# Optimization experiments

Hardware: AMD Instinct MI355X
Metric: run time of the kernel (lower is better)

Reference implementation:

```python
import jax, jax.numpy as jnp
import numpy as np

GROUP_SIZE = 128

def _dequantize(qweight, wscales, wzeros):
    # qweight: [N, K//2] packed bytes, two uint4 values per byte
    # low nibble = even k index, high nibble = odd k index
    N, Kh = qweight.shape
    K = Kh * 2
    low = qweight & 0xF
    high = (qweight >> 4) & 0xF
    w_int = jnp.stack([low, high], axis=-1).reshape(N, K).astype(jnp.float32)  # [N, K]
    G = K // GROUP_SIZE  # number of groups along K
    w_grp = w_int.reshape(N, G, GROUP_SIZE)
    s = wscales.T.reshape(N, G, 1)   # wscales: [G, N] -> [N, G, 1]
    z = wzeros.T.reshape(N, G, 1)
    return ((w_grp - z) * s).reshape(N, K)  # [N, K] dequantized

def setup_inputs() -> dict:
    key = jax.random.key(0)
    k1, k2, k3, k4, k5 = jax.random.split(key, 5)
    M, K, N = 4096, 4096, 12288
    G = K // GROUP_SIZE
    x = jax.random.normal(k1, (M, K), dtype=jnp.float32)
    qweight = jax.random.randint(k2, (N, K // 2), 0, 256, dtype=jnp.int32)
    wscales = jax.random.uniform(k3, (G, N), dtype=jnp.float32) * 0.05
    wzeros = jax.random.uniform(k4, (G, N), dtype=jnp.float32) * 15.0
    bias = jax.random.normal(k5, (N,), dtype=jnp.float32)
    return {"x": x, "qweight": qweight, "wscales": wscales, "wzeros": wzeros, "bias": bias}

def reference(x, qweight, wscales, wzeros, bias):
    # AWQ W4A16 linear: y = x @ dequant(W)^T + b
    w = _dequantize(qweight, wscales, wzeros)  # [N, K]
    return jnp.einsum('mk,nk->mn', x, w) + bias
```

## Files before the change

### kernel.cpp

```cpp
#include <hip/hip_runtime.h>

#define M_DIM 4096
#define K_DIM 4096
#define N_DIM 12288
#define BM 256
#define BN 128
#define BK 64

typedef __bf16 bf16x8  __attribute__((ext_vector_type(8)));
typedef float  floatx16 __attribute__((ext_vector_type(16)));

__global__ __launch_bounds__(256) void xcast_kernel(const float* __restrict__ x,
                                                    __bf16* __restrict__ xb) {
    int idx = blockIdx.x * 256 + threadIdx.x;
    const float4* xv = (const float4*)x;
    float4 a = xv[idx * 2];
    float4 b = xv[idx * 2 + 1];
    bf16x8 o;
    o[0] = (__bf16)a.x; o[1] = (__bf16)a.y; o[2] = (__bf16)a.z; o[3] = (__bf16)a.w;
    o[4] = (__bf16)b.x; o[5] = (__bf16)b.y; o[6] = (__bf16)b.z; o[7] = (__bf16)b.w;
    ((bf16x8*)xb)[idx] = o;
}

__global__ __launch_bounds__(256) void dequant_kernel(const int* __restrict__ qw,
                                                      const float* __restrict__ scales,
                                                      const float* __restrict__ zeros,
                                                      __bf16* __restrict__ wb) {
    int idx = blockIdx.x * 256 + threadIdx.x;
    int n  = idx >> 9;
    int jq = (idx & 511) << 2;
    int g  = jq >> 6;
    float s = scales[g * N_DIM + n];
    float z = zeros[g * N_DIM + n];
    int4 q = *(const int4*)(qw + (size_t)n * (K_DIM / 2) + jq);
    bf16x8 o;
    o[0] = (__bf16)(((float)(q.x & 15)        - z) * s);
    o[1] = (__bf16)(((float)((q.x >> 4) & 15) - z) * s);
    o[2] = (__bf16)(((float)(q.y & 15)        - z) * s);
    o[3] = (__bf16)(((float)((q.y >> 4) & 15) - z) * s);
    o[4] = (__bf16)(((float)(q.z & 15)        - z) * s);
    o[5] = (__bf16)(((float)((q.z >> 4) & 15) - z) * s);
    o[6] = (__bf16)(((float)(q.w & 15)        - z) * s);
    o[7] = (__bf16)(((float)((q.w >> 4) & 15) - z) * s);
    *(bf16x8*)(wb + (size_t)n * K_DIM + (size_t)jq * 2) = o;
}

__global__ __launch_bounds__(256, 2) void gemm_kernel(const __bf16* __restrict__ A,
                                                      const __bf16* __restrict__ B,
                                                      const float* __restrict__ bias,
                                                      float* __restrict__ C) {
    __shared__ __bf16 As[BM * BK];
    __shared__ __bf16 Bs[BN * BK];

    const int tid  = threadIdx.x;
    const int wave = tid >> 6;
    const int lane = tid & 63;
    const int l32  = lane & 31;
    const int half = lane >> 5;
    const int wm = (wave >> 1) * 128;
    const int wn = (wave & 1) * 64;
    const int bm0 = blockIdx.x * BM;
    const int bn0 = blockIdx.y * BN;

    const int rowInChunk = lane >> 3;
    const int slot       = lane & 7;

    const int gread = (l32 & 7) ^ (((l32 >> 3) & 3) << 1);

    floatx16 acc[4][2] = {};

    for (int kt = 0; kt < K_DIM / BK; ++kt) {
        const int k0 = kt * BK;
        #pragma unroll
        for (int r = 0; r < 8; ++r) {
            const int chunk = wave * 8 + r;
            const int row   = chunk * 8 + rowInChunk;
            const int kblk  = slot ^ rowInChunk ^ ((r & 3) << 1);
            const __bf16* ga = A + (size_t)(bm0 + row) * K_DIM + k0 + kblk * 8;
            __builtin_amdgcn_global_load_lds(
                (const __attribute__((address_space(1))) void*)ga,
                (__attribute__((address_space(3))) void*)(As + chunk * 512), 16, 0, 0);
        }
        #pragma unroll
        for (int r = 0; r < 4; ++r) {
            const int chunk = wave * 4 + r;
            const int row   = chunk * 8 + rowInChunk;
            const int kblk  = slot ^ rowInChunk ^ ((r & 3) << 1);
            const __bf16* gb = B + (size_t)(bn0 + row) * K_DIM + k0 + kblk * 8;
            __builtin_amdgcn_global_load_lds(
                (const __attribute__((address_space(1))) void*)gb,
                (__attribute__((address_space(3))) void*)(Bs + chunk * 512), 16, 0, 0);
        }
        __syncthreads();

        #pragma unroll
        for (int ks = 0; ks < 4; ++ks) {
            const int blk = ks * 2 + half;
            const int off = (blk ^ gread) << 3;
            bf16x8 af[4], bfr[2];
            #pragma unroll
            for (int i = 0; i < 4; ++i)
                af[i] = *(const bf16x8*)(As + (wm + i * 32 + l32) * BK + off);
            #pragma unroll
            for (int t = 0; t < 2; ++t)
                bfr[t] = *(const bf16x8*)(Bs + (wn + t * 32 + l32) * BK + off);
            #pragma unroll
            for (int mi = 0; mi < 4; ++mi)
                #pragma unroll
                for (int ni = 0; ni < 2; ++ni)
                    acc[mi][ni] = __builtin_amdgcn_mfma_f32_32x32x16_bf16(
                        af[mi], bfr[ni], acc[mi][ni], 0, 0, 0);
        }
        __syncthreads();
    }

    #pragma unroll
    for (int ni = 0; ni < 2; ++ni) {
        const int col = bn0 + wn + ni * 32 + l32;
        const float bv = bias[col];
        #pragma unroll
        for (int mi = 0; mi < 4; ++mi) {
            #pragma unroll
            for (int reg = 0; reg < 16; ++reg) {
                const int row = bm0 + wm + mi * 32 + half * 4 + (reg & 3) + 8 * (reg >> 2);
                C[(size_t)row * N_DIM + col] = acc[mi][ni][reg] + bv;
            }
        }
    }
}

extern "C" void kernel_launch(void* const* d_in, const int* in_sizes, int n_in,
                              void* d_out, int out_size, void* d_ws, size_t ws_size,
                              hipStream_t stream) {
    const float* x      = (const float*)d_in[0];
    const int*   qw     = (const int*)d_in[1];
    const float* scales = (const float*)d_in[2];
    const float* zeros  = (const float*)d_in[3];
    const float* bias   = (const float*)d_in[4];
    float* out = (float*)d_out;

    __bf16* xb = (__bf16*)d_ws;
    __bf16* wb = (__bf16*)((char*)d_ws + (size_t)M_DIM * K_DIM * 2);

    xcast_kernel<<<(M_DIM * K_DIM / 8) / 256, 256, 0, stream>>>(x, xb);
    dequant_kernel<<<(N_DIM * (K_DIM / 2) / 4) / 256, 256, 0, stream>>>(qw, scales, zeros, wb);

    dim3 grid(M_DIM / BM, N_DIM / BN);
    gemm_kernel<<<grid, 256, 0, stream>>>(xb, wb, bias, out);
}
```

Measured before the change: 683.4 us.

## Double-buffer 256x256 GEMM tile with 8 waves and interleaved load/MFMA phases

The GEMM tile grows to 256x256 and runs with 512 threads (8 waves). LDS is double-buffered so global-to-LDS loads for the next K step are issued in four phases interleaved with MFMA quadrants, with setprio and explicit vmcnt waits. The aim is to hide global load latency and raise arithmetic intensity per block. The cost is more LDS (128KB) and hand-scheduled barriers that could stall or reduce occupancy. The last iteration wraps around and issues a redundant prefetch.

```diff
diff --git a/kernel.cpp b/kernel.cpp
--- a/kernel.cpp
+++ b/kernel.cpp
@@ -4,8 +4,9 @@
 #define K_DIM 4096
 #define N_DIM 12288
 #define BM 256
-#define BN 128
+#define BN 256
 #define BK 64
+#define NT (K_DIM / BK)
 
 typedef __bf16 bf16x8  __attribute__((ext_vector_type(8)));
 typedef float  floatx16 __attribute__((ext_vector_type(16)));
@@ -45,88 +46,147 @@
     *(bf16x8*)(wb + (size_t)n * K_DIM + (size_t)jq * 2) = o;
 }
 
-__global__ __launch_bounds__(256, 2) void gemm_kernel(const __bf16* __restrict__ A,
+__global__ __launch_bounds__(512, 2) void gemm_kernel(const __bf16* __restrict__ A,
                                                       const __bf16* __restrict__ B,
                                                       const float* __restrict__ bias,
                                                       float* __restrict__ C) {
-    __shared__ __bf16 As[BM * BK];
-    __shared__ __bf16 Bs[BN * BK];
+    __shared__ __bf16 As[2][BM * BK];
+    __shared__ __bf16 Bs[2][BN * BK];
 
     const int tid  = threadIdx.x;
     const int wave = tid >> 6;
     const int lane = tid & 63;
     const int l32  = lane & 31;
     const int half = lane >> 5;
-    const int wm = (wave >> 1) * 128;
-    const int wn = (wave & 1) * 64;
-    const int bm0 = blockIdx.x * BM;
-    const int bn0 = blockIdx.y * BN;
+    const int side = wave >> 2;
+    const int aw   = wave & 3;
+    const int wm   = side * 128;
+    const int wn   = aw * 64;
+    const int bm0  = blockIdx.x * BM;
+    const int bn0  = blockIdx.y * BN;
 
     const int rowInChunk = lane >> 3;
     const int slot       = lane & 7;
-
-    const int gread = (l32 & 7) ^ (((l32 >> 3) & 3) << 1);
-
-    floatx16 acc[4][2] = {};
-
-    for (int kt = 0; kt < K_DIM / BK; ++kt) {
-        const int k0 = kt * BK;
-        #pragma unroll
-        for (int r = 0; r < 8; ++r) {
-            const int chunk = wave * 8 + r;
-            const int row   = chunk * 8 + rowInChunk;
-            const int kblk  = slot ^ rowInChunk ^ ((r & 3) << 1);
-            const __bf16* ga = A + (size_t)(bm0 + row) * K_DIM + k0 + kblk * 8;
-            __builtin_amdgcn_global_load_lds(
-                (const __attribute__((address_space(1))) void*)ga,
-                (__attribute__((address_space(3))) void*)(As + chunk * 512), 16, 0, 0);
-        }
-        #pragma unroll
-        for (int r = 0; r < 4; ++r) {
-            const int chunk = wave * 4 + r;
-            const int row   = chunk * 8 + rowInChunk;
-            const int kblk  = slot ^ rowInChunk ^ ((r & 3) << 1);
-            const __bf16* gb = B + (size_t)(bn0 + row) * K_DIM + k0 + kblk * 8;
-            __builtin_amdgcn_global_load_lds(
-                (const __attribute__((address_space(1))) void*)gb,
-                (__attribute__((address_space(3))) void*)(Bs + chunk * 512), 16, 0, 0);
-        }
-        __syncthreads();
-
-        #pragma unroll
-        for (int ks = 0; ks < 4; ++ks) {
-            const int blk = ks * 2 + half;
-            const int off = (blk ^ gread) << 3;
-            bf16x8 af[4], bfr[2];
-            #pragma unroll
-            for (int i = 0; i < 4; ++i)
-                af[i] = *(const bf16x8*)(As + (wm + i * 32 + l32) * BK + off);
-            #pragma unroll
-            for (int t = 0; t < 2; ++t)
-                bfr[t] = *(const bf16x8*)(Bs + (wn + t * 32 + l32) * BK + off);
-            #pragma unroll
-            for (int mi = 0; mi < 4; ++mi)
-                #pragma unroll
-                for (int ni = 0; ni < 2; ++ni)
-                    acc[mi][ni] = __builtin_amdgcn_mfma_f32_32x32x16_bf16(
-                        af[mi], bfr[ni], acc[mi][ni], 0, 0, 0);
-        }
-        __syncthreads();
+    const int gread      = (l32 & 7) ^ (((l32 >> 3) & 3) << 1);
+
+    const int ca0 = side * 16 + aw * 2;
+    const int ca1 = side * 16 + 8 + aw * 2;
+    const int cb  = aw * 8 + side * 4;
+
+    #define SRCKEY(c) (slot ^ rowInChunk ^ (((c) & 3) << 1))
+    const __bf16* sA0 = A + (size_t)(bm0 + (ca0    ) * 8 + rowInChunk) * K_DIM + SRCKEY(ca0    ) * 8;
+    const __bf16* sA1 = A + (size_t)(bm0 + (ca0 + 1) * 8 + rowInChunk) * K_DIM + SRCKEY(ca0 + 1) * 8;
+    const __bf16* sA2 = A + (size_t)(bm0 + (ca1    ) * 8 + rowInChunk) * K_DIM + SRCKEY(ca1    ) * 8;
+    const __bf16* sA3 = A + (size_t)(bm0 + (ca1 + 1) * 8 + rowInChunk) * K_DIM + SRCKEY(ca1 + 1) * 8;
+    const __bf16* sB0 = B + (size_t)(bn0 + (cb     ) * 8 + rowInChunk) * K_DIM + SRCKEY(cb     ) * 8;
+    const __bf16* sB1 = B + (size_t)(bn0 + (cb  + 1) * 8 + rowInChunk) * K_DIM + SRCKEY(cb  + 1) * 8;
+    const __bf16* sB2 = B + (size_t)(bn0 + (cb  + 2) * 8 + rowInChunk) * K_DIM + SRCKEY(cb  + 2) * 8;
+    const __bf16* sB3 = B + (size_t)(bn0 + (cb  + 3) * 8 + rowInChunk) * K_DIM + SRCKEY(cb  + 3) * 8;
+
+    const int dA0 = (ca0    ) * 512, dA1 = (ca0 + 1) * 512;
+    const int dA2 = (ca1    ) * 512, dA3 = (ca1 + 1) * 512;
+    const int dB0 = (cb     ) * 512, dB1 = (cb  + 1) * 512;
+    const int dB2 = (cb  + 2) * 512, dB3 = (cb  + 3) * 512;
+
+    #define GLOAD(G, L) __builtin_amdgcn_global_load_lds( \
+        (const __attribute__((address_space(1))) void*)(G), \
+        (__attribute__((address_space(3))) void*)(L), 16, 0, 0)
+
+    const int rA0 = (wm +  0 + l32) * BK;
+    const int rA1 = (wm + 32 + l32) * BK;
+    const int rA2 = (wm + 64 + l32) * BK;
+    const int rA3 = (wm + 96 + l32) * BK;
+    const int rB0 = (wn +  0 + l32) * BK;
+    const int rB1 = (wn + 32 + l32) * BK;
+    const int ko0 = ((0 * 2 + half) ^ gread) << 3;
+    const int ko1 = ((1 * 2 + half) ^ gread) << 3;
+    const int ko2 = ((2 * 2 + half) ^ gread) << 3;
+    const int ko3 = ((3 * 2 + half) ^ gread) << 3;
+
+    #define RD(P, R, KO) (*(const bf16x8*)((P) + (R) + (KO)))
+    #define MF(AF, BF, ACC) __builtin_amdgcn_mfma_f32_32x32x16_bf16((AF), (BF), (ACC), 0, 0, 0)
+
+    floatx16 acc00 = {}, acc01 = {}, acc10 = {}, acc11 = {};
+    floatx16 acc20 = {}, acc21 = {}, acc30 = {}, acc31 = {};
+
+    GLOAD(sA0, &As[0][dA0]); GLOAD(sA1, &As[0][dA1]);
+    GLOAD(sB0, &Bs[0][dB0]); GLOAD(sB1, &Bs[0][dB1]);
+    GLOAD(sB2, &Bs[0][dB2]); GLOAD(sB3, &Bs[0][dB3]);
+    GLOAD(sA2, &As[0][dA2]); GLOAD(sA3, &As[0][dA3]);
+    asm volatile("s_waitcnt vmcnt(2)" ::: "memory");
+    __builtin_amdgcn_s_barrier();
+
+    for (int kt = 0; kt < NT; ++kt) {
+        const int cur = kt & 1;
+        const int nxt = cur ^ 1;
+        const int k0n = ((kt + 1) & (NT - 1)) * BK;
+        const __bf16* Ac = &As[cur][0];
+        const __bf16* Bc = &Bs[cur][0];
+
+        GLOAD(sA0 + k0n, &As[nxt][dA0]);
+        GLOAD(sA1 + k0n, &As[nxt][dA1]);
+        bf16x8 a0_0 = RD(Ac, rA0, ko0), a0_1 = RD(Ac, rA0, ko1), a0_2 = RD(Ac, rA0, ko2), a0_3 = RD(Ac, rA0, ko3);
+        bf16x8 a1_0 = RD(Ac, rA1, ko0), a1_1 = RD(Ac, rA1, ko1), a1_2 = RD(Ac, rA1, ko2), a1_3 = RD(Ac, rA1, ko3);
+        bf16x8 b0_0 = RD(Bc, rB0, ko0), b0_1 = RD(Bc, rB0, ko1), b0_2 = RD(Bc, rB0, ko2), b0_3 = RD(Bc, rB0, ko3);
+        __builtin_amdgcn_s_barrier();
+        __builtin_amdgcn_s_setprio(1);
+        acc00 = MF(a0_0, b0_0, acc00); acc10 = MF(a1_0, b0_0, acc10);
+        acc00 = MF(a0_1, b0_1, acc00); acc10 = MF(a1_1, b0_1, acc10);
+        acc00 = MF(a0_2, b0_2, acc00); acc10 = MF(a1_2, b0_2, acc10);
+        acc00 = MF(a0_3, b0_3, acc00); acc10 = MF(a1_3, b0_3, acc10);
+        __builtin_amdgcn_s_setprio(0);
+        __builtin_amdgcn_s_barrier();
+
+        GLOAD(sB0 + k0n, &Bs[nxt][dB0]);
+        GLOAD(sB1 + k0n, &Bs[nxt][dB1]);
+        bf16x8 b1_0 = RD(Bc, rB1, ko0), b1_1 = RD(Bc, rB1, ko1), b1_2 = RD(Bc, rB1, ko2), b1_3 = RD(Bc, rB1, ko3);
+        __builtin_amdgcn_s_barrier();
+        __builtin_amdgcn_s_setprio(1);
+        acc01 = MF(a0_0, b1_0, acc01); acc11 = MF(a1_0, b1_0, acc11);
+        acc01 = MF(a0_1, b1_1, acc01); acc11 = MF(a1_1, b1_1, acc11);
+        acc01 = MF(a0_2, b1_2, acc01); acc11 = MF(a1_2, b1_2, acc11);
+        acc01 = MF(a0_3, b1_3, acc01); acc11 = MF(a1_3, b1_3, acc11);
+        __builtin_amdgcn_s_setprio(0);
+        asm volatile("s_waitcnt vmcnt(4)" ::: "memory");
+        __builtin_amdgcn_s_barrier();
+
+        GLOAD(sB2 + k0n, &Bs[nxt][dB2]);
+        GLOAD(sB3 + k0n, &Bs[nxt][dB3]);
+        bf16x8 a2_0 = RD(Ac, rA2, ko0), a2_1 = RD(Ac, rA2, ko1), a2_2 = RD(Ac, rA2, ko2), a2_3 = RD(Ac, rA2, ko3);
+        bf16x8 a3_0 = RD(Ac, rA3, ko0), a3_1 = RD(Ac, rA3, ko1), a3_2 = RD(Ac, rA3, ko2), a3_3 = RD(Ac, rA3, ko3);
+        __builtin_amdgcn_s_barrier();
+        __builtin_amdgcn_s_setprio(1);
+        acc21 = MF(a2_0, b1_0, acc21); acc31 = MF(a3_0, b1_0, acc31);
+        acc21 = MF(a2_1, b1_1, acc21); acc31 = MF(a3_1, b1_1, acc31);
+        acc21 = MF(a2_2, b1_2, acc21); acc31 = MF(a3_2, b1_2, acc31);
+        acc21 = MF(a2_3, b1_3, acc21); acc31 = MF(a3_3, b1_3, acc31);
+        __builtin_amdgcn_s_setprio(0);
+        __builtin_amdgcn_s_barrier();
+
+        GLOAD(sA2 + k0n, &As[nxt][dA2]);
+        GLOAD(sA3 + k0n, &As[nxt][dA3]);
+        __builtin_amdgcn_s_setprio(1);
+        acc20 = MF(a2_0, b0_0, acc20); acc30 = MF(a3_0, b0_0, acc30);
+        acc20 = MF(a2_1, b0_1, acc20); acc30 = MF(a3_1, b0_1, acc30);
+        acc20 = MF(a2_2, b0_2, acc20); acc30 = MF(a3_2, b0_2, acc30);
+        acc20 = MF(a2_3, b0_3, acc20); acc30 = MF(a3_3, b0_3, acc30);
+        __builtin_amdgcn_s_setprio(0);
+        asm volatile("s_waitcnt vmcnt(2)" ::: "memory");
+        __builtin_amdgcn_s_barrier();
     }
 
-    #pragma unroll
-    for (int ni = 0; ni < 2; ++ni) {
-        const int col = bn0 + wn + ni * 32 + l32;
-        const float bv = bias[col];
-        #pragma unroll
-        for (int mi = 0; mi < 4; ++mi) {
-            #pragma unroll
-            for (int reg = 0; reg < 16; ++reg) {
-                const int row = bm0 + wm + mi * 32 + half * 4 + (reg & 3) + 8 * (reg >> 2);
-                C[(size_t)row * N_DIM + col] = acc[mi][ni][reg] + bv;
-            }
-        }
-    }
+    #define EPI(ACC, MI, NI) { \
+        const int col = bn0 + wn + (NI) * 32 + l32; \
+        const float bv = bias[col]; \
+        _Pragma("unroll") \
+        for (int r = 0; r < 16; ++r) { \
+            const int row = bm0 + wm + (MI) * 32 + half * 4 + (r & 3) + 8 * (r >> 2); \
+            C[(size_t)row * N_DIM + col] = ACC[r] + bv; \
+        } }
+    EPI(acc00, 0, 0); EPI(acc01, 0, 1);
+    EPI(acc10, 1, 0); EPI(acc11, 1, 1);
+    EPI(acc20, 2, 0); EPI(acc21, 2, 1);
+    EPI(acc30, 3, 0); EPI(acc31, 3, 1);
 }
 
 extern "C" void kernel_launch(void* const* d_in, const int* in_sizes, int n_in,
@@ -146,5 +206,5 @@
     dequant_kernel<<<(N_DIM * (K_DIM / 2) / 4) / 256, 256, 0, stream>>>(qw, scales, zeros, wb);
 
     dim3 grid(M_DIM / BM, N_DIM / BN);
-    gemm_kernel<<<grid, 256, 0, stream>>>(xb, wb, bias, out);
-}
+    gemm_kernel<<<grid, 512, 0, stream>>>(xb, wb, bias, out);
+}
```

After: 780.1 us. +14.2%, slower.

## Fuse int4 dequantization into GEMM B-tile load and swizzle block order

Applied to the files above, without the earlier changes.

Removes the separate dequant kernel and its bf16 weight buffer. Each GEMM block now reads packed int4 weights into registers one K-tile ahead, dequantizes them, and writes swizzled bf16 straight into shared memory. Block IDs are also remapped so neighbouring blocks share N columns and stay in cache together. In exchange, every M-tile (16 of them) redoes the dequant arithmetic and adds VALU work and register use inside the main loop.

```diff
diff --git a/kernel.cpp b/kernel.cpp
--- a/kernel.cpp
+++ b/kernel.cpp
@@ -6,6 +6,7 @@
 #define BM 256
 #define BN 128
 #define BK 64
+#define NT (K_DIM / BK)
 
 typedef __bf16 bf16x8  __attribute__((ext_vector_type(8)));
 typedef float  floatx16 __attribute__((ext_vector_type(16)));
@@ -22,31 +23,10 @@
     ((bf16x8*)xb)[idx] = o;
 }
 
-__global__ __launch_bounds__(256) void dequant_kernel(const int* __restrict__ qw,
+__global__ __launch_bounds__(256, 2) void gemm_kernel(const __bf16* __restrict__ A,
+                                                      const int* __restrict__ Q,
                                                       const float* __restrict__ scales,
                                                       const float* __restrict__ zeros,
-                                                      __bf16* __restrict__ wb) {
-    int idx = blockIdx.x * 256 + threadIdx.x;
-    int n  = idx >> 9;
-    int jq = (idx & 511) << 2;
-    int g  = jq >> 6;
-    float s = scales[g * N_DIM + n];
-    float z = zeros[g * N_DIM + n];
-    int4 q = *(const int4*)(qw + (size_t)n * (K_DIM / 2) + jq);
-    bf16x8 o;
-    o[0] = (__bf16)(((float)(q.x & 15)        - z) * s);
-    o[1] = (__bf16)(((float)((q.x >> 4) & 15) - z) * s);
-    o[2] = (__bf16)(((float)(q.y & 15)        - z) * s);
-    o[3] = (__bf16)(((float)((q.y >> 4) & 15) - z) * s);
-    o[4] = (__bf16)(((float)(q.z & 15)        - z) * s);
-    o[5] = (__bf16)(((float)((q.z >> 4) & 15) - z) * s);
-    o[6] = (__bf16)(((float)(q.w & 15)        - z) * s);
-    o[7] = (__bf16)(((float)((q.w >> 4) & 15) - z) * s);
-    *(bf16x8*)(wb + (size_t)n * K_DIM + (size_t)jq * 2) = o;
-}
-
-__global__ __launch_bounds__(256, 2) void gemm_kernel(const __bf16* __restrict__ A,
-                                                      const __bf16* __restrict__ B,
                                                       const float* __restrict__ bias,
                                                       float* __restrict__ C) {
     __shared__ __bf16 As[BM * BK];
@@ -59,17 +39,44 @@
     const int half = lane >> 5;
     const int wm = (wave >> 1) * 128;
     const int wn = (wave & 1) * 64;
-    const int bm0 = blockIdx.x * BM;
-    const int bn0 = blockIdx.y * BN;
+
+    const int bid = blockIdx.y * 16 + blockIdx.x;
+    const int sw  = (bid & 7) * 192 + (bid >> 3);
+    const int bm0 = (sw & 15) * BM;
+    const int bn0 = (sw >> 4) * BN;
 
     const int rowInChunk = lane >> 3;
     const int slot       = lane & 7;
+    const int gread      = (l32 & 7) ^ (((l32 >> 3) & 3) << 1);
 
-    const int gread = (l32 & 7) ^ (((l32 >> 3) & 3) << 1);
+    const int brow = tid >> 1;
+    const int hk   = tid & 1;
+    const int gr   = (brow & 7) ^ (((brow >> 3) & 3) << 1);
+    const int ncol = bn0 + brow;
+    const int* qrow = Q + (size_t)ncol * (K_DIM / 2) + hk * 16;
+    __bf16* bdst = Bs + brow * 64;
 
     floatx16 acc[4][2] = {};
 
-    for (int kt = 0; kt < K_DIM / BK; ++kt) {
+    int4 q0 = *(const int4*)(qrow + 0);
+    int4 q1 = *(const int4*)(qrow + 4);
+    int4 q2 = *(const int4*)(qrow + 8);
+    int4 q3 = *(const int4*)(qrow + 12);
+    float scur = scales[ncol];
+    float zcur = zeros[ncol];
+
+    #define DQW(Q4, J) { bf16x8 o; \
+        o[0] = (__bf16)(((float)((Q4).x & 15)        - zcur) * scur); \
+        o[1] = (__bf16)(((float)(((Q4).x >> 4) & 15) - zcur) * scur); \
+        o[2] = (__bf16)(((float)((Q4).y & 15)        - zcur) * scur); \
+        o[3] = (__bf16)(((float)(((Q4).y >> 4) & 15) - zcur) * scur); \
+        o[4] = (__bf16)(((float)((Q4).z & 15)        - zcur) * scur); \
+        o[5] = (__bf16)(((float)(((Q4).z >> 4) & 15) - zcur) * scur); \
+        o[6] = (__bf16)(((float)((Q4).w & 15)        - zcur) * scur); \
+        o[7] = (__bf16)(((float)(((Q4).w >> 4) & 15) - zcur) * scur); \
+        *(bf16x8*)(bdst + (((hk * 4 + (J)) ^ gr) << 3)) = o; }
+
+    for (int kt = 0; kt < NT; ++kt) {
         const int k0 = kt * BK;
         #pragma unroll
         for (int r = 0; r < 8; ++r) {
@@ -81,17 +88,17 @@
                 (const __attribute__((address_space(1))) void*)ga,
                 (__attribute__((address_space(3))) void*)(As + chunk * 512), 16, 0, 0);
         }
-        #pragma unroll
-        for (int r = 0; r < 4; ++r) {
-            const int chunk = wave * 4 + r;
-            const int row   = chunk * 8 + rowInChunk;
-            const int kblk  = slot ^ rowInChunk ^ ((r & 3) << 1);
-            const __bf16* gb = B + (size_t)(bn0 + row) * K_DIM + k0 + kblk * 8;
-            __builtin_amdgcn_global_load_lds(
-                (const __attribute__((address_space(1))) void*)gb,
-                (__attribute__((address_space(3))) void*)(Bs + chunk * 512), 16, 0, 0);
-        }
+        DQW(q0, 0); DQW(q1, 1); DQW(q2, 2); DQW(q3, 3);
         __syncthreads();
+
+        const int kn = (kt + 1) & (NT - 1);
+        const int cb = kn * 32;
+        q0 = *(const int4*)(qrow + cb + 0);
+        q1 = *(const int4*)(qrow + cb + 4);
+        q2 = *(const int4*)(qrow + cb + 8);
+        q3 = *(const int4*)(qrow + cb + 12);
+        scur = scales[(kn >> 1) * N_DIM + ncol];
+        zcur = zeros[(kn >> 1) * N_DIM + ncol];
 
         #pragma unroll
         for (int ks = 0; ks < 4; ++ks) {
@@ -140,11 +147,9 @@
     float* out = (float*)d_out;
 
     __bf16* xb = (__bf16*)d_ws;
-    __bf16* wb = (__bf16*)((char*)d_ws + (size_t)M_DIM * K_DIM * 2);
 
     xcast_kernel<<<(M_DIM * K_DIM / 8) / 256, 256, 0, stream>>>(x, xb);
-    dequant_kernel<<<(N_DIM * (K_DIM / 2) / 4) / 256, 256, 0, stream>>>(qw, scales, zeros, wb);
 
     dim3 grid(M_DIM / BM, N_DIM / BN);
-    gemm_kernel<<<grid, 256, 0, stream>>>(xb, wb, bias, out);
+    gemm_kernel<<<grid, 256, 0, stream>>>(xb, qw, scales, zeros, bias, out);
 }
```

New measurement: 746.4 us. 9.2% more time.
